# Optimization experiments

Hardware: AMD Instinct MI355X
Metric: run time of the kernel (lower is better)

Reference implementation:

```python
import jax, jax.numpy as jnp
import numpy as np
from jax import lax

B = 65536

def _conv(x, w, b):
    y = lax.conv_general_dilated(x, w, (1, 1), 'VALID',
                                 dimension_numbers=('NCHW', 'OIHW', 'NCHW'))
    return y + b[None, :, None, None]

def _maxpool2(x):
    return lax.reduce_window(x, -jnp.inf, lax.max, (1, 1, 2, 2), (1, 1, 2, 2), 'VALID')

def _cnot01(s):  # control wire0, target wire1; s: [B,2,2] indexed [b,q0,q1]
    return jnp.stack([s[:, 0, :], s[:, 1, ::-1]], axis=1)

def _cnot10(s):  # control wire1, target wire0
    return jnp.stack([s[:, :, 0], s[:, ::-1, 1]], axis=2)

def _ry(half_angle):  # RY(2*half_angle) as used in circuit (theta/2 = half_angle)
    c, si = jnp.cos(half_angle), jnp.sin(half_angle)
    return jnp.stack([jnp.stack([c, -si]), jnp.stack([si, c])]).astype(jnp.complex64)

def _apply_w0(s, U):
    return jnp.einsum('ij,bjk->bik', U, s)

def _apply_w1(s, U):
    return jnp.einsum('ij,bkj->bki', U, s)

def _quantum(x2, p):
    # x2: [B,2] float32, p: [8] float32. Batched 2-qubit statevector sim.
    x0, x1 = x2[:, 0], x2[:, 1]
    n = x2.shape[0]
    s = jnp.full((n, 2, 2), 0.5 + 0.0j, dtype=jnp.complex64)  # H|0> x H|0>
    # RZ(2*x0) on wire 0: diag(e^{-i x0}, e^{i x0})
    s = s * jnp.exp(1j * jnp.stack([-x0, x0], axis=1).astype(jnp.complex64))[:, :, None]
    # RZ(2*x1) on wire 1
    s = s * jnp.exp(1j * jnp.stack([-x1, x1], axis=1).astype(jnp.complex64))[:, None, :]
    s = _cnot01(s)
    ang = (jnp.pi - x0) * (jnp.pi - x1)  # RZ(2*ang) on wire 1
    s = s * jnp.exp(1j * jnp.stack([-ang, ang], axis=1).astype(jnp.complex64))[:, None, :]
    s = _cnot01(s)
    s = _apply_w0(s, _ry(p[0])); s = _apply_w1(s, _ry(p[1])); s = _cnot01(s)
    s = _apply_w0(s, _ry(p[2])); s = _apply_w1(s, _ry(p[3])); s = _cnot10(s)
    s = _apply_w0(s, _ry(p[4])); s = _apply_w1(s, _ry(p[5])); s = _cnot01(s)
    s = _apply_w0(s, _ry(p[6])); s = _apply_w1(s, _ry(p[7]))
    z = jnp.array([[1.0, -1.0], [-1.0, 1.0]], dtype=jnp.float32)  # Z0 (x) Z1 signs
    prob = (s.real ** 2 + s.imag ** 2)
    return jnp.sum(prob * z[None], axis=(1, 2))  # [B]

def setup_inputs() -> dict:
    key = jax.random.key(0)
    ks = jax.random.split(key, 12)
    d = {}
    d['x'] = jax.random.normal(ks[0], (B, 1, 28, 28), dtype=jnp.float32)
    d['conv1_w'] = jax.random.normal(ks[1], (2, 1, 5, 5), dtype=jnp.float32) * 0.2
    d['conv1_b'] = jax.random.normal(ks[2], (2,), dtype=jnp.float32) * 0.1
    d['conv2_w'] = jax.random.normal(ks[3], (16, 2, 5, 5), dtype=jnp.float32) * 0.14
    d['conv2_b'] = jax.random.normal(ks[4], (16,), dtype=jnp.float32) * 0.1
    d['fc1_w'] = jax.random.normal(ks[5], (64, 256), dtype=jnp.float32) * 0.0625
    d['fc1_b'] = jax.random.normal(ks[6], (64,), dtype=jnp.float32) * 0.05
    d['fc2_w'] = jax.random.normal(ks[7], (2, 64), dtype=jnp.float32) * 0.125
    d['fc2_b'] = jax.random.normal(ks[8], (2,), dtype=jnp.float32) * 0.05
    d['fc3_w'] = jax.random.normal(ks[9], (1, 1), dtype=jnp.float32)
    d['fc3_b'] = jax.random.normal(ks[10], (1,), dtype=jnp.float32) * 0.05
    d['qnn_params'] = jax.random.uniform(ks[11], (8,), dtype=jnp.float32)
    return d

def reference(x, conv1_w, conv1_b, conv2_w, conv2_b, fc1_w, fc1_b,
              fc2_w, fc2_b, fc3_w, fc3_b, qnn_params):
    h = jax.nn.relu(_conv(x, conv1_w, conv1_b))        # [B,2,24,24]
    h = _maxpool2(h)                                    # [B,2,12,12]
    h = jax.nn.relu(_conv(h, conv2_w, conv2_b))        # [B,16,8,8]
    h = _maxpool2(h)                                    # [B,16,4,4]
    # Dropout2d: identity in eval mode
    h = h.reshape(h.shape[0], -1)                       # [B,256]
    h = jax.nn.relu(h @ fc1_w.T + fc1_b)                # [B,64]
    h = h @ fc2_w.T + fc2_b                             # [B,2]
    q = _quantum(h, qnn_params)[:, None]                # [B,1]
    y = q @ fc3_w.T + fc3_b                             # [B,1]
    logits = jnp.concatenate([y, 1.0 - y], axis=-1)     # [B,2]
    return jax.nn.log_softmax(logits, axis=1)
```

## Files before the change

kernel.cpp:

```cpp
#include <hip/hip_runtime.h>
#include <math.h>


typedef float v2f __attribute__((ext_vector_type(2)));
typedef float f32x4 __attribute__((ext_vector_type(4)));
typedef short bf16x8 __attribute__((ext_vector_type(8)));
typedef unsigned int u32x4 __attribute__((ext_vector_type(4)));

union B8 { unsigned int u[4]; bf16x8 v; };

static __device__ __forceinline__ v2f vmax2(v2f a, v2f b) {
    return __builtin_elementwise_max(a, b);
}

#define PK_FMA_W0(acc, w, xp) \
    asm("v_pk_fma_f32 %0, %1, %2, %0 op_sel:[0,0,0] op_sel_hi:[1,0,1]" \
        : "+v"(acc) : "s"(w), "v"(xp))
#define PK_FMA_W1(acc, w, xp) \
    asm("v_pk_fma_f32 %0, %1, %2, %0 op_sel:[0,1,0] op_sel_hi:[1,1,1]" \
        : "+v"(acc) : "s"(w), "v"(xp))

#define MFMA16(a, b, c) __builtin_amdgcn_mfma_f32_16x16x32_bf16(a, b, c, 0, 0, 0)

#define SEL_HI 0x07060302u
#define SEL_LO 0x05040100u

static __device__ __forceinline__ unsigned int pack1(float v) {
    unsigned int hi = __float_as_uint(v) & 0xFFFF0000u;
    float lo = v - __uint_as_float(hi);
    return hi | (__float_as_uint(lo) >> 16);
}

#define A2_HI 0
#define A2_LO 1536
#define A1_HI 3072
#define A1_LO (3072 + 16384)

#define P1_S 296
#define HB_S 260

__global__ __launch_bounds__(256)
void hqcnn_prep(const float* __restrict__ w2, const float* __restrict__ fw1,
                unsigned short* __restrict__ ws) {
    int t = blockIdx.x * 256 + threadIdx.x;
    if (blockIdx.x == 0) {
        for (int e = threadIdx.x; e < 1536; e += 256) {
            int cc = e >> 9, r = e & 511;
            int lid = r >> 3, j = r & 7;
            int nn = lid & 15, qq = lid >> 4;
            int row = cc * 4 + qq;
            int ch = (row >= 5) ? 1 : 0;
            int u = row - 5 * ch;
            float val = (row < 10 && j < 5) ? w2[nn * 50 + ch * 25 + u * 5 + j] : 0.f;
            unsigned int uu = __float_as_uint(val);
            float lo = val - __uint_as_float(uu & 0xFFFF0000u);
            ws[A2_HI + e] = (unsigned short)(uu >> 16);
            ws[A2_LO + e] = (unsigned short)(__float_as_uint(lo) >> 16);
        }
    }
    for (int e = t; e < 16384; e += gridDim.x * 256) {
        int m = e >> 8, kp = e & 255;
        int oc = kp & 15, s16 = kp >> 4;
        float val = fw1[m * 256 + oc * 16 + s16];
        unsigned int u = __float_as_uint(val);
        float lo = val - __uint_as_float(u & 0xFFFF0000u);
        ws[A1_HI + e] = (unsigned short)(u >> 16);
        ws[A1_LO + e] = (unsigned short)(__float_as_uint(lo) >> 16);
    }
}

__global__ __launch_bounds__(256, 6)
void hqcnn_fused(const float* __restrict__ x,
                 const float* __restrict__ w1,
                 const float* __restrict__ b1,
                 const float* __restrict__ b2,
                 const float* __restrict__ fb1,
                 const float* __restrict__ fw2,
                 const float* __restrict__ fb2,
                 const float* __restrict__ fw3,
                 const float* __restrict__ fb3,
                 const float* __restrict__ qp,
                 const unsigned short* __restrict__ ws,
                 float* __restrict__ out)
{
    __shared__ __align__(16) unsigned int p1u[8 * P1_S];
    __shared__ __align__(16) unsigned int hbu[8 * HB_S];
    __shared__ __align__(16) float zbuf[4 * 32];

    const int t = threadIdx.x;
    const int wv = t >> 6;
    const int lane = t & 63;
    const int n = lane & 15;
    const int q = lane >> 4;
    const long base = (long)blockIdx.x * 8;

    if (t < 64)
        p1u[(t >> 3) * P1_S + 288 + (t & 7)] = 0u;

    {
        v2f w1p[25];
        #pragma unroll
        for (int k = 0; k < 25; ++k)
            w1p[k] = (v2f){w1[k], w1[25 + k]};
        const v2f bias1 = (v2f){b1[0], b1[1]};

        #pragma unroll
        for (int it = 0; it < 2; ++it) {
            int f = t + it * 256;
            if (f < 384) {
                int s = f / 48;
                int r = f - s * 48;
                int i = r >> 2, jh = r & 3;
                const float* xrow = x + (base + s) * 784;
                v2f acc[12];
                #pragma unroll
                for (int qq = 0; qq < 12; ++qq) acc[qq] = (v2f){0.f, 0.f};
                #pragma unroll
                for (int u = 0; u < 6; ++u) {
                    const v2f* xp = (const v2f*)(xrow + (2 * i + u) * 28 + 6 * jh);
                    v2f P[5] = { xp[0], xp[1], xp[2], xp[3], xp[4] };
                    #pragma unroll
                    for (int a = 0; a < 2; ++a) {
                        if (a <= u && (u - a) <= 4) {
                            const int wu = u - a;
                            #pragma unroll
                            for (int v = 0; v < 5; ++v) {
                                #pragma unroll
                                for (int j = 0; j < 6; ++j) {
                                    const int e = j + v;
                                    if (e & 1) { PK_FMA_W1(acc[a * 6 + j], w1p[wu * 5 + v], P[e >> 1]); }
                                    else       { PK_FMA_W0(acc[a * 6 + j], w1p[wu * 5 + v], P[e >> 1]); }
                                }
                            }
                        }
                    }
                }
                #pragma unroll
                for (int m = 0; m < 3; ++m) {
                    v2f mx = vmax2(vmax2(acc[2 * m], acc[2 * m + 1]),
                                   vmax2(acc[6 + 2 * m], acc[7 + 2 * m]));
                    mx = mx + bias1;
                    mx = vmax2(mx, (v2f){0.f, 0.f});
                    int pc = 3 * jh + m;
                    int off = s * P1_S + i * 12 + pc;
                    p1u[off] = pack1(mx.x);
                    p1u[off + 144] = pack1(mx.y);
                }
            }
        }
    }
    __syncthreads();

    {
        const bf16x8* B2h = (const bf16x8*)(ws + A2_HI);
        const bf16x8* B2l = (const bf16x8*)(ws + A2_LO);
        bf16x8 b_h[3], b_l[3];
        #pragma unroll
        for (int cc = 0; cc < 3; ++cc) {
            b_h[cc] = B2h[cc * 64 + lane];
            b_l[cc] = B2l[cc * 64 + lane];
        }
        const int quad = n >> 2;
        const int di = (n >> 1) & 1;
        const int dj = n & 1;
        const int scol = 2 * quad + dj;
        int chu[3];
        #pragma unroll
        for (int cc = 0; cc < 3; ++cc) {
            int row = cc * 4 + q;
            int ch = (row >= 5) ? 1 : 0;
            int u = row - 5 * ch;
            chu[cc] = (row < 10) ? (ch * 144 + u * 12) : -1;
        }
        const float bias = b2[n];

        #pragma unroll 2
        for (int t8 = 0; t8 < 8; ++t8) {
            int smp = 2 * wv + (t8 >> 2);
            int tt = t8 & 3;
            int pbase = smp * P1_S + (2 * tt + di) * 12 + scol;
            int zaddr = smp * P1_S + 288;
            f32x4 acc = {0.f, 0.f, 0.f, 0.f};
            f32x4 acc2 = {0.f, 0.f, 0.f, 0.f};
            #pragma unroll
            for (int cc = 0; cc < 3; ++cc) {
                int a = (chu[cc] >= 0) ? (pbase + chu[cc]) : zaddr;
                unsigned int e0 = p1u[a],     e1 = p1u[a + 1], e2 = p1u[a + 2],
                             e3 = p1u[a + 3], e4 = p1u[a + 4];
                B8 AH, AL;
                AH.u[0] = __builtin_amdgcn_perm(e1, e0, SEL_HI);
                AH.u[1] = __builtin_amdgcn_perm(e3, e2, SEL_HI);
                AH.u[2] = e4 >> 16;
                AH.u[3] = 0u;
                AL.u[0] = __builtin_amdgcn_perm(e1, e0, SEL_LO);
                AL.u[1] = __builtin_amdgcn_perm(e3, e2, SEL_LO);
                AL.u[2] = e4 & 0xFFFFu;
                AL.u[3] = 0u;
                acc  = MFMA16(AH.v, b_h[cc], acc);
                acc2 = MFMA16(AL.v, b_h[cc], acc2);
                acc  = MFMA16(AH.v, b_l[cc], acc);
            }
            acc = acc + acc2;
            float pv = fmaxf(fmaxf(acc[0], acc[1]), fmaxf(acc[2], acc[3]));
            pv = fmaxf(pv + bias, 0.f);
            hbu[smp * HB_S + (tt * 4 + q) * 16 + n] = pack1(pv);
        }
    }
    __syncthreads();

    {
        const bf16x8* A1h = (const bf16x8*)(ws + A1_HI);
        const bf16x8* A1l = (const bf16x8*)(ws + A1_LO);
        const int abase = (wv * 16 + n) * 32 + q;
        f32x4 acc = {0.f, 0.f, 0.f, 0.f};
        f32x4 acc2 = {0.f, 0.f, 0.f, 0.f};
        #pragma unroll
        for (int kk = 0; kk < 8; ++kk) {
            bf16x8 ah = A1h[abase + kk * 4];
            bf16x8 al = A1l[abase + kk * 4];
            B8 BH, BL;
            if (n < 8) {
                const u32x4* hp = (const u32x4*)(hbu + n * HB_S + kk * 32 + q * 8);
                u32x4 d0 = hp[0], d1 = hp[1];
                BH.u[0] = __builtin_amdgcn_perm(d0.y, d0.x, SEL_HI);
                BH.u[1] = __builtin_amdgcn_perm(d0.w, d0.z, SEL_HI);
                BH.u[2] = __builtin_amdgcn_perm(d1.y, d1.x, SEL_HI);
                BH.u[3] = __builtin_amdgcn_perm(d1.w, d1.z, SEL_HI);
                BL.u[0] = __builtin_amdgcn_perm(d0.y, d0.x, SEL_LO);
                BL.u[1] = __builtin_amdgcn_perm(d0.w, d0.z, SEL_LO);
                BL.u[2] = __builtin_amdgcn_perm(d1.y, d1.x, SEL_LO);
                BL.u[3] = __builtin_amdgcn_perm(d1.w, d1.z, SEL_LO);
            } else {
                BH.u[0] = BH.u[1] = BH.u[2] = BH.u[3] = 0u;
                BL.u[0] = BL.u[1] = BL.u[2] = BL.u[3] = 0u;
            }
            acc  = MFMA16(ah, BH.v, acc);
            acc2 = MFMA16(ah, BL.v, acc2);
            acc  = MFMA16(al, BH.v, acc);
        }
        acc = acc + acc2;
        f32x4 fb4 = *(const f32x4*)(fb1 + wv * 16 + q * 4);
        f32x4 w20 = *(const f32x4*)(fw2 + wv * 16 + q * 4);
        f32x4 w21 = *(const f32x4*)(fw2 + 64 + wv * 16 + q * 4);
        float p0 = 0.f, p1v = 0.f;
        #pragma unroll
        for (int r = 0; r < 4; ++r) {
            float a = fmaxf(acc[r] + fb4[r], 0.f);
            p0  = fmaf(a, w20[r], p0);
            p1v = fmaf(a, w21[r], p1v);
        }
        p0  += __shfl_xor(p0, 16, 64);  p0  += __shfl_xor(p0, 32, 64);
        p1v += __shfl_xor(p1v, 16, 64); p1v += __shfl_xor(p1v, 32, 64);
        if (q == 0) {
            zbuf[wv * 32 + n * 2]     = p0;
            zbuf[wv * 32 + n * 2 + 1] = p1v;
        }
    }
    __syncthreads();

    {
        int s = t & 7;
        float x0 = fb2[0] + zbuf[s * 2]     + zbuf[32 + s * 2]
                          + zbuf[64 + s * 2] + zbuf[96 + s * 2];
        float x1 = fb2[1] + zbuf[s * 2 + 1] + zbuf[32 + s * 2 + 1]
                          + zbuf[64 + s * 2 + 1] + zbuf[96 + s * 2 + 1];

        float sr[4], si[4];
        {
            float th0 = -x0 - x1, th1 = -x0 + x1, th2 = x0 - x1, th3 = x0 + x1;
            sr[0] = 0.5f * __cosf(th0); si[0] = 0.5f * __sinf(th0);
            sr[1] = 0.5f * __cosf(th1); si[1] = 0.5f * __sinf(th1);
            sr[2] = 0.5f * __cosf(th2); si[2] = 0.5f * __sinf(th2);
            sr[3] = 0.5f * __cosf(th3); si[3] = 0.5f * __sinf(th3);
        }
        {
            float tr = sr[2]; sr[2] = sr[3]; sr[3] = tr;
            float ti = si[2]; si[2] = si[3]; si[3] = ti;
            float ang = ((float)M_PI - x0) * ((float)M_PI - x1);
            float ca = __cosf(ang), sa = __sinf(ang);
            float r, im;
            r = sr[0]; im = si[0]; sr[0] = r*ca + im*sa; si[0] = im*ca - r*sa;
            r = sr[2]; im = si[2]; sr[2] = r*ca + im*sa; si[2] = im*ca - r*sa;
            r = sr[1]; im = si[1]; sr[1] = r*ca - im*sa; si[1] = im*ca + r*sa;
            r = sr[3]; im = si[3]; sr[3] = r*ca - im*sa; si[3] = im*ca + r*sa;
            tr = sr[2]; sr[2] = sr[3]; sr[3] = tr;
            ti = si[2]; si[2] = si[3]; si[3] = ti;
        }
        float cp[8], sp[8];
        #pragma unroll
        for (int g = 0; g < 8; ++g) { float qv = qp[g]; cp[g] = __cosf(qv); sp[g] = __sinf(qv); }

        #define QRY0(cc, ss) { \
            float a0r=sr[0], a0i=si[0], a1r=sr[2], a1i=si[2]; \
            sr[0]=cc*a0r-ss*a1r; si[0]=cc*a0i-ss*a1i; \
            sr[2]=ss*a0r+cc*a1r; si[2]=ss*a0i+cc*a1i; \
            float b0r=sr[1], b0i=si[1], b1r=sr[3], b1i=si[3]; \
            sr[1]=cc*b0r-ss*b1r; si[1]=cc*b0i-ss*b1i; \
            sr[3]=ss*b0r+cc*b1r; si[3]=ss*b0i+cc*b1i; }
        #define QRY1(cc, ss) { \
            float a0r=sr[0], a0i=si[0], a1r=sr[1], a1i=si[1]; \
            sr[0]=cc*a0r-ss*a1r; si[0]=cc*a0i-ss*a1i; \
            sr[1]=ss*a0r+cc*a1r; si[1]=ss*a0i+cc*a1i; \
            float b0r=sr[2], b0i=si[2], b1r=sr[3], b1i=si[3]; \
            sr[2]=cc*b0r-ss*b1r; si[2]=cc*b0i-ss*b1i; \
            sr[3]=ss*b0r+cc*b1r; si[3]=ss*b0i+cc*b1i; }
        #define QSWAP(i_, j_) { float tr=sr[i_]; sr[i_]=sr[j_]; sr[j_]=tr; \
                                float ti=si[i_]; si[i_]=si[j_]; si[j_]=ti; }

        QRY0(cp[0], sp[0]);
        QRY1(cp[1], sp[1]);
        QSWAP(2, 3);
        QRY0(cp[2], sp[2]);
        QRY1(cp[3], sp[3]);
        QSWAP(1, 3);
        QRY0(cp[4], sp[4]);
        QRY1(cp[5], sp[5]);
        QSWAP(2, 3);
        QRY0(cp[6], sp[6]);
        QRY1(cp[7], sp[7]);

        float qv = (sr[0]*sr[0] + si[0]*si[0])
                 - (sr[1]*sr[1] + si[1]*si[1])
                 - (sr[2]*sr[2] + si[2]*si[2])
                 + (sr[3]*sr[3] + si[3]*si[3]);
        float y = fmaf(qv, fw3[0], fb3[0]);
        float l0 = y, l1 = 1.0f - y;
        float m = fmaxf(l0, l1);
        float lse = m + __logf(__expf(l0 - m) + __expf(l1 - m));
        if (t < 16) {
            int comp = t >> 3;
            out[(base + s) * 2 + comp] = comp ? (l1 - lse) : (l0 - lse);
        }
        #undef QRY0
        #undef QRY1
        #undef QSWAP
    }
}

extern "C" void kernel_launch(void* const* d_in, const int* in_sizes, int n_in,
                              void* d_out, int out_size, void* d_ws, size_t ws_size,
                              hipStream_t stream) {
    const float* x   = (const float*)d_in[0];
    const float* w1  = (const float*)d_in[1];
    const float* b1  = (const float*)d_in[2];
    const float* w2  = (const float*)d_in[3];
    const float* b2  = (const float*)d_in[4];
    const float* fw1 = (const float*)d_in[5];
    const float* fb1 = (const float*)d_in[6];
    const float* fw2 = (const float*)d_in[7];
    const float* fb2 = (const float*)d_in[8];
    const float* fw3 = (const float*)d_in[9];
    const float* fb3 = (const float*)d_in[10];
    const float* qp  = (const float*)d_in[11];
    float* outp = (float*)d_out;
    unsigned short* wsp = (unsigned short*)d_ws;

    hipLaunchKernelGGL(hqcnn_prep, dim3(64), dim3(256), 0, stream, w2, fw1, wsp);

    int B = in_sizes[0] / 784;
    int nblk = B / 8;
    hipLaunchKernelGGL(hqcnn_fused, dim3(nblk), dim3(256), 0, stream,
                       x, w1, b1, b2, fb1, fw2, fb2, fw3, fb3, qp, wsp, outp);
}
```

Measured before the change: 385.9 us.

## Process 16 samples per block and reuse pool buffer for conv2 output

Doubles the samples per block from 8 to 16 so the fc1 MFMA, whose N dimension is 16, has no zero-padded columns. The conv2 pooled outputs are now written back into the p1 shared buffer in place of a separate hb buffer, which keeps the LDS footprint small and allows launch bounds to request 8 blocks per CU. Each wave handles 4 samples and buffers its results in registers before overwriting its own slice. The quantum tail now runs in only one wave, with 16 samples per wave. The risks are higher register pressure under the stricter occupancy bound and fewer blocks in the grid.

```diff
diff --git a/kernel.cpp b/kernel.cpp
--- a/kernel.cpp
+++ b/kernel.cpp
@@ -36,8 +36,7 @@
 #define A1_HI 3072
 #define A1_LO (3072 + 16384)
 
-#define P1_S 296
-#define HB_S 260
+#define P1_S 300
 
 __global__ __launch_bounds__(256)
 void hqcnn_prep(const float* __restrict__ w2, const float* __restrict__ fw1,
@@ -69,7 +68,7 @@
     }
 }
 
-__global__ __launch_bounds__(256, 6)
+__global__ __launch_bounds__(256, 8)
 void hqcnn_fused(const float* __restrict__ x,
                  const float* __restrict__ w1,
                  const float* __restrict__ b1,
@@ -83,8 +82,7 @@
                  const unsigned short* __restrict__ ws,
                  float* __restrict__ out)
 {
-    __shared__ __align__(16) unsigned int p1u[8 * P1_S];
-    __shared__ __align__(16) unsigned int hbu[8 * HB_S];
+    __shared__ __align__(16) unsigned int p1u[16 * P1_S];
     __shared__ __align__(16) float zbuf[4 * 32];
 
     const int t = threadIdx.x;
@@ -92,9 +90,9 @@
     const int lane = t & 63;
     const int n = lane & 15;
     const int q = lane >> 4;
-    const long base = (long)blockIdx.x * 8;
-
-    if (t < 64)
+    const long base = (long)blockIdx.x * 16;
+
+    if (t < 128)
         p1u[(t >> 3) * P1_S + 288 + (t & 7)] = 0u;
 
     {
@@ -105,47 +103,45 @@
         const v2f bias1 = (v2f){b1[0], b1[1]};
 
         #pragma unroll
-        for (int it = 0; it < 2; ++it) {
+        for (int it = 0; it < 3; ++it) {
             int f = t + it * 256;
-            if (f < 384) {
-                int s = f / 48;
-                int r = f - s * 48;
-                int i = r >> 2, jh = r & 3;
-                const float* xrow = x + (base + s) * 784;
-                v2f acc[12];
+            int s = f / 48;
+            int r = f - s * 48;
+            int i = r >> 2, jh = r & 3;
+            const float* xrow = x + (base + s) * 784;
+            v2f acc[12];
+            #pragma unroll
+            for (int qq = 0; qq < 12; ++qq) acc[qq] = (v2f){0.f, 0.f};
+            #pragma unroll
+            for (int u = 0; u < 6; ++u) {
+                const v2f* xp = (const v2f*)(xrow + (2 * i + u) * 28 + 6 * jh);
+                v2f P[5] = { xp[0], xp[1], xp[2], xp[3], xp[4] };
                 #pragma unroll
-                for (int qq = 0; qq < 12; ++qq) acc[qq] = (v2f){0.f, 0.f};
-                #pragma unroll
-                for (int u = 0; u < 6; ++u) {
-                    const v2f* xp = (const v2f*)(xrow + (2 * i + u) * 28 + 6 * jh);
-                    v2f P[5] = { xp[0], xp[1], xp[2], xp[3], xp[4] };
-                    #pragma unroll
-                    for (int a = 0; a < 2; ++a) {
-                        if (a <= u && (u - a) <= 4) {
-                            const int wu = u - a;
+                for (int a = 0; a < 2; ++a) {
+                    if (a <= u && (u - a) <= 4) {
+                        const int wu = u - a;
+                        #pragma unroll
+                        for (int v = 0; v < 5; ++v) {
                             #pragma unroll
-                            for (int v = 0; v < 5; ++v) {
-                                #pragma unroll
-                                for (int j = 0; j < 6; ++j) {
-                                    const int e = j + v;
-                                    if (e & 1) { PK_FMA_W1(acc[a * 6 + j], w1p[wu * 5 + v], P[e >> 1]); }
-                                    else       { PK_FMA_W0(acc[a * 6 + j], w1p[wu * 5 + v], P[e >> 1]); }
-                                }
+                            for (int j = 0; j < 6; ++j) {
+                                const int e = j + v;
+                                if (e & 1) { PK_FMA_W1(acc[a * 6 + j], w1p[wu * 5 + v], P[e >> 1]); }
+                                else       { PK_FMA_W0(acc[a * 6 + j], w1p[wu * 5 + v], P[e >> 1]); }
                             }
                         }
                     }
                 }
-                #pragma unroll
-                for (int m = 0; m < 3; ++m) {
-                    v2f mx = vmax2(vmax2(acc[2 * m], acc[2 * m + 1]),
-                                   vmax2(acc[6 + 2 * m], acc[7 + 2 * m]));
-                    mx = mx + bias1;
-                    mx = vmax2(mx, (v2f){0.f, 0.f});
-                    int pc = 3 * jh + m;
-                    int off = s * P1_S + i * 12 + pc;
-                    p1u[off] = pack1(mx.x);
-                    p1u[off + 144] = pack1(mx.y);
-                }
+            }
+            #pragma unroll
+            for (int m = 0; m < 3; ++m) {
+                v2f mx = vmax2(vmax2(acc[2 * m], acc[2 * m + 1]),
+                               vmax2(acc[6 + 2 * m], acc[7 + 2 * m]));
+                mx = mx + bias1;
+                mx = vmax2(mx, (v2f){0.f, 0.f});
+                int pc = 3 * jh + m;
+                int off = s * P1_S + i * 12 + pc;
+                p1u[off] = pack1(mx.x);
+                p1u[off + 144] = pack1(mx.y);
             }
         }
     }
@@ -174,36 +170,41 @@
         }
         const float bias = b2[n];
 
-        #pragma unroll 2
-        for (int t8 = 0; t8 < 8; ++t8) {
-            int smp = 2 * wv + (t8 >> 2);
-            int tt = t8 & 3;
-            int pbase = smp * P1_S + (2 * tt + di) * 12 + scol;
-            int zaddr = smp * P1_S + 288;
-            f32x4 acc = {0.f, 0.f, 0.f, 0.f};
-            f32x4 acc2 = {0.f, 0.f, 0.f, 0.f};
-            #pragma unroll
-            for (int cc = 0; cc < 3; ++cc) {
-                int a = (chu[cc] >= 0) ? (pbase + chu[cc]) : zaddr;
-                unsigned int e0 = p1u[a],     e1 = p1u[a + 1], e2 = p1u[a + 2],
-                             e3 = p1u[a + 3], e4 = p1u[a + 4];
-                B8 AH, AL;
-                AH.u[0] = __builtin_amdgcn_perm(e1, e0, SEL_HI);
-                AH.u[1] = __builtin_amdgcn_perm(e3, e2, SEL_HI);
-                AH.u[2] = e4 >> 16;
-                AH.u[3] = 0u;
-                AL.u[0] = __builtin_amdgcn_perm(e1, e0, SEL_LO);
-                AL.u[1] = __builtin_amdgcn_perm(e3, e2, SEL_LO);
-                AL.u[2] = e4 & 0xFFFFu;
-                AL.u[3] = 0u;
-                acc  = MFMA16(AH.v, b_h[cc], acc);
-                acc2 = MFMA16(AL.v, b_h[cc], acc2);
-                acc  = MFMA16(AH.v, b_l[cc], acc);
+        for (int sp = 0; sp < 4; ++sp) {
+            const int smp = 4 * wv + sp;
+            const int sbase = smp * P1_S;
+            const int zaddr = sbase + 288;
+            float pvv[4];
+            #pragma unroll
+            for (int tt = 0; tt < 4; ++tt) {
+                int pbase = sbase + (2 * tt + di) * 12 + scol;
+                f32x4 acc = {0.f, 0.f, 0.f, 0.f};
+                f32x4 acc2 = {0.f, 0.f, 0.f, 0.f};
+                #pragma unroll
+                for (int cc = 0; cc < 3; ++cc) {
+                    int a = (chu[cc] >= 0) ? (pbase + chu[cc]) : zaddr;
+                    unsigned int e0 = p1u[a],     e1 = p1u[a + 1], e2 = p1u[a + 2],
+                                 e3 = p1u[a + 3], e4 = p1u[a + 4];
+                    B8 AH, AL;
+                    AH.u[0] = __builtin_amdgcn_perm(e1, e0, SEL_HI);
+                    AH.u[1] = __builtin_amdgcn_perm(e3, e2, SEL_HI);
+                    AH.u[2] = e4 >> 16;
+                    AH.u[3] = 0u;
+                    AL.u[0] = __builtin_amdgcn_perm(e1, e0, SEL_LO);
+                    AL.u[1] = __builtin_amdgcn_perm(e3, e2, SEL_LO);
+                    AL.u[2] = e4 & 0xFFFFu;
+                    AL.u[3] = 0u;
+                    acc  = MFMA16(AH.v, b_h[cc], acc);
+                    acc2 = MFMA16(AL.v, b_h[cc], acc2);
+                    acc  = MFMA16(AH.v, b_l[cc], acc);
+                }
+                acc = acc + acc2;
+                float pv = fmaxf(fmaxf(acc[0], acc[1]), fmaxf(acc[2], acc[3]));
+                pvv[tt] = fmaxf(pv + bias, 0.f);
             }
-            acc = acc + acc2;
-            float pv = fmaxf(fmaxf(acc[0], acc[1]), fmaxf(acc[2], acc[3]));
-            pv = fmaxf(pv + bias, 0.f);
-            hbu[smp * HB_S + (tt * 4 + q) * 16 + n] = pack1(pv);
+            #pragma unroll
+            for (int tt = 0; tt < 4; ++tt)
+                p1u[sbase + tt * 64 + lane] = pack1(pvv[tt]);
         }
     }
     __syncthreads();
@@ -218,22 +219,17 @@
         for (int kk = 0; kk < 8; ++kk) {
             bf16x8 ah = A1h[abase + kk * 4];
             bf16x8 al = A1l[abase + kk * 4];
+            const u32x4* hp = (const u32x4*)(p1u + n * P1_S + kk * 32 + q * 8);
+            u32x4 d0 = hp[0], d1 = hp[1];
             B8 BH, BL;
-            if (n < 8) {
-                const u32x4* hp = (const u32x4*)(hbu + n * HB_S + kk * 32 + q * 8);
-                u32x4 d0 = hp[0], d1 = hp[1];
-                BH.u[0] = __builtin_amdgcn_perm(d0.y, d0.x, SEL_HI);
-                BH.u[1] = __builtin_amdgcn_perm(d0.w, d0.z, SEL_HI);
-                BH.u[2] = __builtin_amdgcn_perm(d1.y, d1.x, SEL_HI);
-                BH.u[3] = __builtin_amdgcn_perm(d1.w, d1.z, SEL_HI);
-                BL.u[0] = __builtin_amdgcn_perm(d0.y, d0.x, SEL_LO);
-                BL.u[1] = __builtin_amdgcn_perm(d0.w, d0.z, SEL_LO);
-                BL.u[2] = __builtin_amdgcn_perm(d1.y, d1.x, SEL_LO);
-                BL.u[3] = __builtin_amdgcn_perm(d1.w, d1.z, SEL_LO);
-            } else {
-                BH.u[0] = BH.u[1] = BH.u[2] = BH.u[3] = 0u;
-                BL.u[0] = BL.u[1] = BL.u[2] = BL.u[3] = 0u;
-            }
+            BH.u[0] = __builtin_amdgcn_perm(d0.y, d0.x, SEL_HI);
+            BH.u[1] = __builtin_amdgcn_perm(d0.w, d0.z, SEL_HI);
+            BH.u[2] = __builtin_amdgcn_perm(d1.y, d1.x, SEL_HI);
+            BH.u[3] = __builtin_amdgcn_perm(d1.w, d1.z, SEL_HI);
+            BL.u[0] = __builtin_amdgcn_perm(d0.y, d0.x, SEL_LO);
+            BL.u[1] = __builtin_amdgcn_perm(d0.w, d0.z, SEL_LO);
+            BL.u[2] = __builtin_amdgcn_perm(d1.y, d1.x, SEL_LO);
+            BL.u[3] = __builtin_amdgcn_perm(d1.w, d1.z, SEL_LO);
             acc  = MFMA16(ah, BH.v, acc);
             acc2 = MFMA16(ah, BL.v, acc2);
             acc  = MFMA16(al, BH.v, acc);
@@ -257,9 +253,10 @@
         }
     }
     __syncthreads();
+    if (wv != 0) return;
 
     {
-        int s = t & 7;
+        int s = lane & 15;
         float x0 = fb2[0] + zbuf[s * 2]     + zbuf[32 + s * 2]
                           + zbuf[64 + s * 2] + zbuf[96 + s * 2];
         float x1 = fb2[1] + zbuf[s * 2 + 1] + zbuf[32 + s * 2 + 1]
@@ -327,8 +324,8 @@
         float l0 = y, l1 = 1.0f - y;
         float m = fmaxf(l0, l1);
         float lse = m + __logf(__expf(l0 - m) + __expf(l1 - m));
-        if (t < 16) {
-            int comp = t >> 3;
+        if (lane < 32) {
+            int comp = lane >> 4;
             out[(base + s) * 2 + comp] = comp ? (l1 - lse) : (l0 - lse);
         }
         #undef QRY0
@@ -358,7 +355,7 @@
     hipLaunchKernelGGL(hqcnn_prep, dim3(64), dim3(256), 0, stream, w2, fw1, wsp);
 
     int B = in_sizes[0] / 784;
-    int nblk = B / 8;
+    int nblk = B / 16;
     hipLaunchKernelGGL(hqcnn_fused, dim3(nblk), dim3(256), 0, stream,
                        x, w1, b1, b2, fb1, fw2, fb2, fw3, fb3, qp, wsp, outp);
 }
```

New measurement: 370.8 us. -3.9%, faster.
